# Optimization experiments

Measured on AMD Instinct MI355X. Metric: run time of the kernel, lower is better.

Reference implementation:

```python
import jax, jax.numpy as jnp
import numpy as np

B, N, C_IN, G = 8, 65536, 16, 64
CH = [16, 16]
EPS = 1e-3  # keras BatchNormalization default epsilon
OFFSETS = [(dx, dy, dz) for dx in (-1, 0, 1) for dy in (-1, 0, 1) for dz in (-1, 0, 1)]
G3 = G * G * G


def setup_inputs() -> dict:
    key = jax.random.key(0)
    k = jax.random.split(key, 8)
    voxel_features = jax.random.normal(k[0], (B, N, C_IN), dtype=jnp.float32)
    # unique active voxel coordinates per example (submanifold sites)
    lin = jax.vmap(lambda kk: jax.random.permutation(kk, G3)[:N])(jax.random.split(k[1], B))
    xyz = jnp.stack([lin // (G * G), (lin // G) % G, lin % G], axis=-1).astype(jnp.int32)
    num_valid_voxels = jax.random.randint(k[2], (B,), N // 2, N + 1).astype(jnp.int32)
    w0 = jax.random.uniform(k[3], (3, 3, 3, C_IN, CH[0]), minval=-0.05, maxval=0.05, dtype=jnp.float32)
    w1 = jax.random.uniform(k[4], (3, 3, 3, CH[0], CH[1]), minval=-0.05, maxval=0.05, dtype=jnp.float32)
    nw0 = jax.random.uniform(k[5], (3, 3, 3, 1, 1), minval=-0.05, maxval=0.05, dtype=jnp.float32)
    nw1 = jax.random.uniform(k[6], (3, 3, 3, 1, 1), minval=-0.05, maxval=0.05, dtype=jnp.float32)
    gamma0 = jnp.ones((CH[0],), jnp.float32); beta0 = jnp.zeros((CH[0],), jnp.float32)
    gamma1 = jnp.ones((CH[1],), jnp.float32); beta1 = jnp.zeros((CH[1],), jnp.float32)
    return dict(voxel_features=voxel_features, voxel_xyz_indices=xyz,
                num_valid_voxels=num_valid_voxels, w0=w0, w1=w1, nw0=nw0, nw1=nw1,
                gamma0=gamma0, beta0=beta0, gamma1=gamma1, beta1=beta1)


def build_neighbor_idx(coords, valid_mask):
    """For each voxel and each 3x3x3 offset, the row index of the active neighbor, or -1."""
    lin = coords[..., 0] * (G * G) + coords[..., 1] * G + coords[..., 2]  # [B,N]
    # invalid (padded) voxels write to a spare slot so they never match as neighbors
    write_lin = jnp.where(valid_mask, lin, G3 + 1)
    idx_map = jnp.full((B, G3 + 2), -1, jnp.int32)
    idx_map = idx_map.at[jnp.arange(B)[:, None], write_lin].set(
        jnp.broadcast_to(jnp.arange(N, dtype=jnp.int32)[None, :], (B, N)))
    brow = jnp.arange(B)[:, None]
    nb = []
    for dx, dy, dz in OFFSETS:
        nx = coords[..., 0] + dx; ny = coords[..., 1] + dy; nz = coords[..., 2] + dz
        inb = (nx >= 0) & (nx < G) & (ny >= 0) & (ny < G) & (nz >= 0) & (nz < G)
        nlin = jnp.where(inb, nx * (G * G) + ny * G + nz, G3)  # slot G3 always -1
        nb.append(idx_map[brow, nlin])
    return jnp.stack(nb, axis=1)  # [B,27,N]


def sparse_conv(feats, nb_idx, valid_mask, w):
    """Submanifold sparse 3D conv: output only at active sites, gathering active neighbors."""
    wf = w.reshape(27, w.shape[3], w.shape[4])  # offsets enumerate kernel taps in order
    out = jnp.zeros((feats.shape[0], feats.shape[1], w.shape[4]), feats.dtype)
    for o in range(27):
        idx = nb_idx[:, o]  # [B,N]
        g = jnp.take_along_axis(feats, jnp.maximum(idx, 0)[..., None], axis=1)
        g = jnp.where((idx >= 0)[..., None], g, 0.0)
        out = out + jnp.einsum('bnc,co->bno', g, wf[o])
    return out * valid_mask[..., None]


def masked_bn(x, valid_mask, num_valid, gamma, beta):
    m = valid_mask[..., None].astype(x.dtype)
    cnt = jnp.sum(num_valid).astype(x.dtype)
    mean = jnp.sum(x * m, axis=(0, 1)) / cnt
    var = jnp.sum(m * jnp.square(x - mean), axis=(0, 1)) / cnt
    xn = (x - mean) * jax.lax.rsqrt(var + EPS) * gamma + beta
    return xn * m  # padded rows are zero-padded, as in the TF layer


def reference(voxel_features, voxel_xyz_indices, num_valid_voxels,
              w0, w1, nw0, nw1, gamma0, beta0, gamma1, beta1):
    valid_mask = jnp.arange(N)[None, :] < num_valid_voxels[:, None]  # [B,N]
    nb_idx = build_neighbor_idx(voxel_xyz_indices, valid_mask)
    ones = jnp.ones((B, N, 1), jnp.float32)
    net = voxel_features
    for w, nw, g, b in ((w0, nw0, gamma0, beta0), (w1, nw1, gamma1, beta1)):
        net = sparse_conv(net, nb_idx, valid_mask, w)
        net_norm = sparse_conv(ones, nb_idx, valid_mask, nw)
        net = net / (1.0 + jnp.abs(net_norm))
        net = masked_bn(net, valid_mask, num_valid_voxels, g, b)
        net = jax.nn.relu(net)
    return net
```

## Files before the change

kernel.cpp:

```cpp
#include <hip/hip_runtime.h>
#include <cstdint>
#include <cstddef>

#define NB 8
#define NN 65536
#define NS (NN + 16)
#define GG 64
#define GG3 (GG*GG*GG)
#define NW (GG3/32)
#define NBLKC 2048
#define NP32 (NB * 2048)
#define EPSC 1e-3f

typedef __bf16 bf16x8 __attribute__((ext_vector_type(8)));
typedef float  f32x4  __attribute__((ext_vector_type(4)));

__device__ __forceinline__ unsigned short f2bf(float f) {
    unsigned u = __builtin_bit_cast(unsigned, f);
    unsigned r = (u + 0x7fffu + ((u >> 16) & 1u)) >> 16;
    return (unsigned short)r;
}
__device__ __forceinline__ unsigned pk2(float a, float b) {
    return (unsigned)f2bf(a) | ((unsigned)f2bf(b) << 16);
}
__device__ __forceinline__ float bf2f(unsigned short s) {
    return __builtin_bit_cast(float, (unsigned)s << 16);
}

__device__ __forceinline__ int site_rank2(const int2* __restrict__ mwb, int lin) {
    int2 mw = mwb[lin >> 5];
    uint32_t w = (uint32_t)mw.x;
    uint32_t bit = 1u << (lin & 31);
    if (!(w & bit)) return -1;
    return mw.y + __popc(w & (bit - 1u));
}

__global__ __launch_bounds__(256) void build_mask_kernel(
    const int* __restrict__ xyz, const int* __restrict__ nvv,
    uint32_t* __restrict__ mask,
    const float* __restrict__ w0, const float* __restrict__ w1,
    unsigned short* __restrict__ wf)
{
    int b = blockIdx.y;
    int n = blockIdx.x * 256 + threadIdx.x;
    if (n < nvv[b]) {
        const int* cp = xyz + ((size_t)b * NN + n) * 3;
        int lin = cp[0] * (GG * GG) + cp[1] * GG + cp[2];
        atomicOr(&mask[b * NW + (lin >> 5)], 1u << (lin & 31));
    }
    if (blockIdx.x == 0 && b < 2) {
        const float* w = b ? w1 : w0;
        unsigned short* o = wf + b * 14 * 512;
        for (int idx = threadIdx.x; idx < 14 * 512; idx += 256) {
            int i = idx >> 9;
            int rem = idx & 511;
            int L = rem >> 3, j = rem & 7;
            int quad = L >> 4, nn = L & 15;
            int off = 2 * i + (quad >> 1);
            int c = ((quad & 1) << 3) + j;
            float v = (off < 27) ? w[(off * 16 + c) * 16 + nn] : 0.f;
            o[idx] = f2bf(v);
        }
    }
}

__global__ __launch_bounds__(256) void scan_mask_kernel(
    const uint32_t* __restrict__ mask, int2* __restrict__ mwb)
{
    int b = blockIdx.x;
    const uint32_t* mb = mask + (size_t)b * NW;
    int2* wb = mwb + (size_t)b * NW;
    int t = threadIdx.x;

    uint32_t wv[32];
    int cnts[32];
    int local = 0;
    #pragma unroll
    for (int i = 0; i < 32; i++) {
        wv[i] = mb[t * 32 + i];
        cnts[i] = __popc(wv[i]);
        local += cnts[i];
    }

    __shared__ int sc[256];
    sc[t] = local;
    __syncthreads();
    for (int off = 1; off < 256; off <<= 1) {
        int v = (t >= off) ? sc[t - off] : 0;
        __syncthreads();
        sc[t] += v;
        __syncthreads();
    }
    int base = sc[t] - local;
    #pragma unroll
    for (int i = 0; i < 32; i++) {
        wb[t * 32 + i] = make_int2((int)wv[i], base);
        base += cnts[i];
    }
}

__global__ __launch_bounds__(256) void perm_gather_kernel(
    const int* __restrict__ xyz, const int* __restrict__ nvv,
    const int2* __restrict__ mwb,
    const float* __restrict__ feats,
    int2* __restrict__ srow,
    unsigned short* __restrict__ sfeats)
{
    int b = blockIdx.y;
    int n = blockIdx.x * 256 + threadIdx.x;
    int cnt = nvv[b];
    unsigned short* sfb = sfeats + (size_t)b * NS * 16;
    if (blockIdx.x == 0 && threadIdx.x < 16)
        sfb[(size_t)NN * 16 + threadIdx.x] = 0;
    if (n < cnt) {
        const int* cp = xyz + ((size_t)b * NN + n) * 3;
        int lin = cp[0] * (GG * GG) + cp[1] * GG + cp[2];
        int r = site_rank2(mwb + (size_t)b * NW, lin);
        srow[(size_t)b * NN + r] = make_int2(lin, n);
        const float4* fp = (const float4*)(feats + ((size_t)b * NN + n) * 16);
        float4 f0 = fp[0], f1 = fp[1], f2 = fp[2], f3 = fp[3];
        uint4 lo = make_uint4(pk2(f0.x, f0.y), pk2(f0.z, f0.w),
                              pk2(f1.x, f1.y), pk2(f1.z, f1.w));
        uint4 hi = make_uint4(pk2(f2.x, f2.y), pk2(f2.z, f2.w),
                              pk2(f3.x, f3.y), pk2(f3.z, f3.w));
        *(uint4*)(sfb + (size_t)r * 16)     = lo;
        *(uint4*)(sfb + (size_t)r * 16 + 8) = hi;
    } else {
        uint4 z = make_uint4(0, 0, 0, 0);
        *(uint4*)(sfb + (size_t)n * 16)     = z;
        *(uint4*)(sfb + (size_t)n * 16 + 8) = z;
    }
}

__global__ __launch_bounds__(256, 4) void conv_mfma_kernel(
    const unsigned short* __restrict__ sfeats,
    const int2*     __restrict__ srow,
    const int*      __restrict__ nvv,
    const int2*     __restrict__ mwb,
    const unsigned short* __restrict__ wfrag,
    const float*    __restrict__ nw,
    unsigned short* __restrict__ outbuf,
    float*          __restrict__ stats)
{
    int lane = threadIdx.x & 63;
    int wv = threadIdx.x >> 6;
    int m = lane & 15, quad = lane >> 4;
    int v = lane & 31, h = lane >> 5;
    int wid = blockIdx.x * 4 + wv;

    __shared__ int   jj[4][32][29];
    __shared__ float obuf[4][32][17];
    __shared__ float rrl[4][32];
    __shared__ float red[4][32];
    __shared__ float lnw[27];

    if (threadIdx.x < 27) lnw[threadIdx.x] = nw[threadIdx.x];

    bf16x8 bfr[14];
    #pragma unroll
    for (int i = 0; i < 14; i++)
        bfr[i] = *(const bf16x8*)(wfrag + i * 512 + lane * 8);
    __syncthreads();

    float psum = 0.f, psq = 0.f;
    int coff = (quad & 1) << 3;

    for (int pb = wid; pb < NP32; pb += 4 * NBLKC) {
        int b = pb >> 11;
        int r0 = (pb & 2047) << 5;
        int cnt = nvv[b];
        if (r0 >= cnt) continue;

        const int2* mb = mwb + (size_t)b * NW;
        const unsigned short* fb = sfeats + (size_t)b * NS * 16;
        const int2* sr = srow + (size_t)b * NN;

        int Rv = r0 + v;
        bool vld = Rv < cnt;
        int lin = vld ? sr[Rv].x : 0;
        int x = lin >> 12, y = (lin >> 6) & 63, z = lin & 63;
        int zb = z & 31;
        float nc = 0.f;
        #pragma unroll
        for (int t = 0; t < 5; t++) {
            int c = 2 * t + h;
            bool cok = c < 9;
            int cc = cok ? c : 0;
            int dx = cc / 3 - 1, dy = cc % 3 - 1;
            int nx = x + dx, ny = y + dy;
            bool colok = cok & ((unsigned)nx < 64u) & ((unsigned)ny < 64u);
            int wdi = colok ? (((nx << 12) + (ny << 6) + z) >> 5) : 0;

            int2 mw = make_int2(0, 0);
            if (vld & colok) mw = mb[wdi];
            bool need2 = vld & colok & (((zb == 0) & (z > 0)) | ((zb == 31) & (z < 63)));
            int w2 = wdi + ((zb == 0) ? -1 : 1);
            int2 mw2 = make_int2(0, 0);
            if (need2) mw2 = mb[w2];

            #pragma unroll
            for (int dz = -1; dz <= 1; dz++) {
                int zz = z + dz;
                bool zok = (unsigned)zz < 64u;
                bool same = (dz == 0) | ((dz < 0) ? (zb != 0) : (zb != 31));
                int2 word = same ? mw : mw2;
                int bb = zz & 31;
                uint32_t wm = (uint32_t)word.x;
                bool hit = vld & colok & zok & ((wm >> bb) & 1u);
                int rnk = word.y + __popc(wm & ((1u << bb) - 1u));
                int off = cc * 3 + dz + 1;
                int jv = hit ? rnk : NN;
                if (cok) {
                    jj[wv][v][off] = jv;
                    nc += hit ? lnw[off] : 0.f;
                }
            }
        }
        nc += __shfl_xor(nc, 32, 64);
        if (lane < 32) rrl[wv][v] = 1.f / (1.f + fabsf(nc));

        f32x4 acc0 = {0.f, 0.f, 0.f, 0.f};
        f32x4 acc1 = {0.f, 0.f, 0.f, 0.f};
        #pragma unroll
        for (int i = 0; i < 14; i++) {
            int off = 2 * i + (quad >> 1);
            int idx = off < 27 ? off : 28;
            int j0 = jj[wv][m][idx];      j0 = (off < 27) ? j0 : NN;
            int j1 = jj[wv][m + 16][idx]; j1 = (off < 27) ? j1 : NN;
            bf16x8 a0 = *(const bf16x8*)(fb + (size_t)j0 * 16 + coff);
            bf16x8 a1 = *(const bf16x8*)(fb + (size_t)j1 * 16 + coff);
            acc0 = __builtin_amdgcn_mfma_f32_16x16x32_bf16(a0, bfr[i], acc0, 0, 0, 0);
            acc1 = __builtin_amdgcn_mfma_f32_16x16x32_bf16(a1, bfr[i], acc1, 0, 0, 0);
        }

        #pragma unroll
        for (int hh = 0; hh < 2; hh++) {
            #pragma unroll
            for (int r4 = 0; r4 < 4; r4++) {
                int row = (hh << 4) + (quad << 2) + r4;
                float tval = (hh ? acc1[r4] : acc0[r4]) * rrl[wv][row];
                psum += tval; psq += tval * tval;
                obuf[wv][row][m] = tval;
            }
        }
        {
            int orow = v;
            int Rr = r0 + orow;
            if (Rr < cnt) {
                const float* src = &obuf[wv][orow][h * 8];
                uint4 val = make_uint4(pk2(src[0], src[1]), pk2(src[2], src[3]),
                                       pk2(src[4], src[5]), pk2(src[6], src[7]));
                *(uint4*)(outbuf + ((size_t)b * NN + Rr) * 16 + h * 8) = val;
            }
        }
    }

    psum += __shfl_xor(psum, 16, 64); psum += __shfl_xor(psum, 32, 64);
    psq  += __shfl_xor(psq, 16, 64);  psq  += __shfl_xor(psq, 32, 64);
    if (lane < 16) { red[wv][lane] = psum; red[wv][16 + lane] = psq; }
    __syncthreads();
    if (threadIdx.x < 32) {
        float vv = red[0][threadIdx.x] + red[1][threadIdx.x] +
                   red[2][threadIdx.x] + red[3][threadIdx.x];
        atomicAdd(&stats[(blockIdx.x & 15) * 32 + threadIdx.x], vv);
    }
}

__device__ __forceinline__ void compute_sb(
    const float* __restrict__ stats, const int* __restrict__ nvv,
    const float* __restrict__ gamma, const float* __restrict__ beta,
    float* sbs , float* sums )
{
    int tid = threadIdx.x;
    if (tid < 32) {
        float v = 0.f;
        #pragma unroll
        for (int s = 0; s < 16; s++) v += stats[s * 32 + tid];
        sums[tid] = v;
    }
    __syncthreads();
    if (tid < 16) {
        float cnt = 0.f;
        #pragma unroll
        for (int b = 0; b < NB; b++) cnt += (float)nvv[b];
        float mean = sums[tid] / cnt;
        float var  = fmaxf(sums[16 + tid] / cnt - mean * mean, 0.f);
        float scv = gamma[tid] * rsqrtf(var + EPSC);
        sbs[tid]      = scv;
        sbs[16 + tid] = beta[tid] - mean * scv;
    }
    __syncthreads();
}

__global__ __launch_bounds__(256) void bnrelu_sorted_kernel(
    const unsigned short* __restrict__ in, const float* __restrict__ stats,
    const int* __restrict__ nvv,
    const float* __restrict__ gamma, const float* __restrict__ beta,
    unsigned short* __restrict__ outb)
{
    __shared__ float sbs[32];
    __shared__ float sums[32];
    compute_sb(stats, nvv, gamma, beta, sbs, sums);

    int b = blockIdx.y;
    int r = blockIdx.x * 256 + threadIdx.x;
    if (r > NN) return;
    int cnt = nvv[b];
    uint4 lo = make_uint4(0, 0, 0, 0), hi = lo;
    if (r < cnt) {
        const uint4* ip = (const uint4*)(in + ((size_t)b * NN + r) * 16);
        uint4 xl = ip[0], xh = ip[1];
        float y[16];
        #pragma unroll
        for (int c = 0; c < 16; c++) {
            unsigned u = (c < 8) ? ((const unsigned*)&xl)[c >> 1]
                                 : ((const unsigned*)&xh)[(c - 8) >> 1];
            unsigned short sv = (c & 1) ? (unsigned short)(u >> 16)
                                        : (unsigned short)(u & 0xffff);
            y[c] = fmaxf(fmaf(bf2f(sv), sbs[c], sbs[16 + c]), 0.f);
        }
        lo = make_uint4(pk2(y[0], y[1]), pk2(y[2], y[3]), pk2(y[4], y[5]), pk2(y[6], y[7]));
        hi = make_uint4(pk2(y[8], y[9]), pk2(y[10], y[11]), pk2(y[12], y[13]), pk2(y[14], y[15]));
    }
    unsigned short* op = outb + ((size_t)b * NS + r) * 16;
    *(uint4*)op       = lo;
    *(uint4*)(op + 8) = hi;
}

__global__ __launch_bounds__(256) void final_scatter_kernel(
    const unsigned short* __restrict__ in,
    const int2* __restrict__ srow,
    const float* __restrict__ stats, const int* __restrict__ nvv,
    const float* __restrict__ gamma, const float* __restrict__ beta,
    float* __restrict__ out)
{
    __shared__ float sbs[32];
    __shared__ float sums[32];
    compute_sb(stats, nvv, gamma, beta, sbs, sums);

    int b = blockIdx.y;
    int r = blockIdx.x * 256 + threadIdx.x;
    int cnt = nvv[b];
    if (r < cnt) {
        const uint4* ip = (const uint4*)(in + ((size_t)b * NN + r) * 16);
        uint4 xl = ip[0], xh = ip[1];
        float y[16];
        #pragma unroll
        for (int c = 0; c < 16; c++) {
            unsigned u = (c < 8) ? ((const unsigned*)&xl)[c >> 1]
                                 : ((const unsigned*)&xh)[(c - 8) >> 1];
            unsigned short sv = (c & 1) ? (unsigned short)(u >> 16)
                                        : (unsigned short)(u & 0xffff);
            y[c] = fmaxf(fmaf(bf2f(sv), sbs[c], sbs[16 + c]), 0.f);
        }
        int n = srow[(size_t)b * NN + r].y;
        float4* op = (float4*)(out + ((size_t)b * NN + n) * 16);
        op[0] = make_float4(y[0],  y[1],  y[2],  y[3]);
        op[1] = make_float4(y[4],  y[5],  y[6],  y[7]);
        op[2] = make_float4(y[8],  y[9],  y[10], y[11]);
        op[3] = make_float4(y[12], y[13], y[14], y[15]);
    } else {
        float4 z = make_float4(0.f, 0.f, 0.f, 0.f);
        float4* op = (float4*)(out + ((size_t)b * NN + r) * 16);
        op[0] = z; op[1] = z; op[2] = z; op[3] = z;
    }
}

extern "C" void kernel_launch(void* const* d_in, const int* in_sizes, int n_in,
                              void* d_out, int out_size, void* d_ws, size_t ws_size,
                              hipStream_t stream)
{
    const float* feats  = (const float*)d_in[0];
    const int*   xyz    = (const int*)d_in[1];
    const int*   nvv    = (const int*)d_in[2];
    const float* w0     = (const float*)d_in[3];
    const float* w1     = (const float*)d_in[4];
    const float* nw0    = (const float*)d_in[5];
    const float* nw1    = (const float*)d_in[6];
    const float* gamma0 = (const float*)d_in[7];
    const float* beta0  = (const float*)d_in[8];
    const float* gamma1 = (const float*)d_in[9];
    const float* beta1  = (const float*)d_in[10];
    float* out = (float*)d_out;

    char* ws = (char*)d_ws;
    uint32_t* mask    = (uint32_t*)ws;       ws += (size_t)NB * NW * 4;
    float*    stats1  = (float*)ws;          ws += 16 * 32 * 4;
    float*    stats2  = (float*)ws;          ws += 16 * 32 * 4;
    int2*     mwb     = (int2*)ws;           ws += (size_t)NB * NW * 8;
    int2*     srow    = (int2*)ws;           ws += (size_t)NB * NN * 8;
    unsigned short* sfA = (unsigned short*)ws; ws += (size_t)NB * NS * 16 * 2;
    unsigned short* sfB = (unsigned short*)ws; ws += (size_t)NB * NS * 16 * 2;
    unsigned short* bufPre = (unsigned short*)ws; ws += (size_t)NB * NN * 16 * 2;
    unsigned short* wfr = (unsigned short*)ws; ws += (size_t)2 * 14 * 512 * 2;

    hipMemsetAsync(mask, 0, (size_t)NB * NW * 4 + 16 * 32 * 4 * 2, stream);

    dim3 gridBN(NN / 256, NB);
    build_mask_kernel<<<gridBN, 256, 0, stream>>>(xyz, nvv, mask, w0, w1, wfr);
    scan_mask_kernel<<<NB, 256, 0, stream>>>(mask, mwb);
    perm_gather_kernel<<<gridBN, 256, 0, stream>>>(xyz, nvv, mwb, feats, srow, sfA);

    conv_mfma_kernel<<<NBLKC, 256, 0, stream>>>(
        sfA, srow, nvv, mwb, wfr, nw0, bufPre, stats1);
    bnrelu_sorted_kernel<<<dim3(NN / 256 + 1, NB), 256, 0, stream>>>(
        bufPre, stats1, nvv, gamma0, beta0, sfB);

    conv_mfma_kernel<<<NBLKC, 256, 0, stream>>>(
        sfB, srow, nvv, mwb, wfr + 14 * 512, nw1, bufPre, stats2);

    final_scatter_kernel<<<dim3(NN / 256, NB), 256, 0, stream>>>(
        bufPre, srow, stats2, nvv, gamma1, beta1, out);
}
```

Measured before the change: 241.0 us.

## Compact conv work list over valid rows and make BN in place

The conv kernel now iterates over a compacted list of only the valid 32-row tiles across batches, using prefix sums of per-batch counts, and runs on a smaller grid. Before, it strided over all tiles and skipped the empty ones, which left waves idle. Linear coordinates are computed once in build_mask and reused by the gather step. The separate pre-BN buffer is dropped: conv writes into the ping-pong buffers, BN+ReLU runs in place, and the zero padding writes for invalid rows are removed, since only the sentinel row at NN is zeroed now. This relies on gathered neighbour indices never touching rows at or beyond the count except the sentinel.

```diff
diff --git a/kernel.cpp b/kernel.cpp
--- a/kernel.cpp
+++ b/kernel.cpp
@@ -8,8 +8,7 @@
 #define GG 64
 #define GG3 (GG*GG*GG)
 #define NW (GG3/32)
-#define NBLKC 2048
-#define NP32 (NB * 2048)
+#define NBLKC 1536
 #define EPSC 1e-3f
 
 typedef __bf16 bf16x8 __attribute__((ext_vector_type(8)));
@@ -37,7 +36,7 @@
 
 __global__ __launch_bounds__(256) void build_mask_kernel(
     const int* __restrict__ xyz, const int* __restrict__ nvv,
-    uint32_t* __restrict__ mask,
+    uint32_t* __restrict__ mask, int* __restrict__ linb,
     const float* __restrict__ w0, const float* __restrict__ w1,
     unsigned short* __restrict__ wf)
 {
@@ -46,6 +45,7 @@
     if (n < nvv[b]) {
         const int* cp = xyz + ((size_t)b * NN + n) * 3;
         int lin = cp[0] * (GG * GG) + cp[1] * GG + cp[2];
+        linb[(size_t)b * NN + n] = lin;
         atomicOr(&mask[b * NW + (lin >> 5)], 1u << (lin & 31));
     }
     if (blockIdx.x == 0 && b < 2) {
@@ -100,7 +100,7 @@
 }
 
 __global__ __launch_bounds__(256) void perm_gather_kernel(
-    const int* __restrict__ xyz, const int* __restrict__ nvv,
+    const int* __restrict__ linb, const int* __restrict__ nvv,
     const int2* __restrict__ mwb,
     const float* __restrict__ feats,
     int2* __restrict__ srow,
@@ -113,8 +113,7 @@
     if (blockIdx.x == 0 && threadIdx.x < 16)
         sfb[(size_t)NN * 16 + threadIdx.x] = 0;
     if (n < cnt) {
-        const int* cp = xyz + ((size_t)b * NN + n) * 3;
-        int lin = cp[0] * (GG * GG) + cp[1] * GG + cp[2];
+        int lin = linb[(size_t)b * NN + n];
         int r = site_rank2(mwb + (size_t)b * NW, lin);
         srow[(size_t)b * NN + r] = make_int2(lin, n);
         const float4* fp = (const float4*)(feats + ((size_t)b * NN + n) * 16);
@@ -125,10 +124,6 @@
                               pk2(f3.x, f3.y), pk2(f3.z, f3.w));
         *(uint4*)(sfb + (size_t)r * 16)     = lo;
         *(uint4*)(sfb + (size_t)r * 16 + 8) = hi;
-    } else {
-        uint4 z = make_uint4(0, 0, 0, 0);
-        *(uint4*)(sfb + (size_t)n * 16)     = z;
-        *(uint4*)(sfb + (size_t)n * 16 + 8) = z;
     }
 }
 
@@ -156,6 +151,15 @@
 
     if (threadIdx.x < 27) lnw[threadIdx.x] = nw[threadIdx.x];
 
+    int cnts[8], cum[9];
+    cum[0] = 0;
+    #pragma unroll
+    for (int b = 0; b < 8; b++) {
+        cnts[b] = nvv[b];
+        cum[b + 1] = cum[b] + ((cnts[b] + 31) >> 5);
+    }
+    int total = cum[8];
+
     bf16x8 bfr[14];
     #pragma unroll
     for (int i = 0; i < 14; i++)
@@ -165,11 +169,12 @@
     float psum = 0.f, psq = 0.f;
     int coff = (quad & 1) << 3;
 
-    for (int pb = wid; pb < NP32; pb += 4 * NBLKC) {
-        int b = pb >> 11;
-        int r0 = (pb & 2047) << 5;
-        int cnt = nvv[b];
-        if (r0 >= cnt) continue;
+    for (int vp = wid; vp < total; vp += 4 * NBLKC) {
+        int b = 0;
+        #pragma unroll
+        for (int k = 1; k < 8; k++) b += (vp >= cum[k]);
+        int r0 = (vp - cum[b]) << 5;
+        int cnt = cnts[b];
 
         const int2* mb = mwb + (size_t)b * NW;
         const unsigned short* fb = sfeats + (size_t)b * NS * 16;
@@ -244,13 +249,12 @@
             }
         }
         {
-            int orow = v;
-            int Rr = r0 + orow;
+            int Rr = r0 + v;
             if (Rr < cnt) {
-                const float* src = &obuf[wv][orow][h * 8];
+                const float* src = &obuf[wv][v][h * 8];
                 uint4 val = make_uint4(pk2(src[0], src[1]), pk2(src[2], src[3]),
                                        pk2(src[4], src[5]), pk2(src[6], src[7]));
-                *(uint4*)(outbuf + ((size_t)b * NN + Rr) * 16 + h * 8) = val;
+                *(uint4*)(outbuf + ((size_t)b * NS + Rr) * 16 + h * 8) = val;
             }
         }
     }
@@ -293,10 +297,9 @@
 }
 
 __global__ __launch_bounds__(256) void bnrelu_sorted_kernel(
-    const unsigned short* __restrict__ in, const float* __restrict__ stats,
+    unsigned short* __restrict__ buf, const float* __restrict__ stats,
     const int* __restrict__ nvv,
-    const float* __restrict__ gamma, const float* __restrict__ beta,
-    unsigned short* __restrict__ outb)
+    const float* __restrict__ gamma, const float* __restrict__ beta)
 {
     __shared__ float sbs[32];
     __shared__ float sums[32];
@@ -306,10 +309,9 @@
     int r = blockIdx.x * 256 + threadIdx.x;
     if (r > NN) return;
     int cnt = nvv[b];
-    uint4 lo = make_uint4(0, 0, 0, 0), hi = lo;
+    unsigned short* op = buf + ((size_t)b * NS + r) * 16;
     if (r < cnt) {
-        const uint4* ip = (const uint4*)(in + ((size_t)b * NN + r) * 16);
-        uint4 xl = ip[0], xh = ip[1];
+        uint4 xl = *(const uint4*)op, xh = *(const uint4*)(op + 8);
         float y[16];
         #pragma unroll
         for (int c = 0; c < 16; c++) {
@@ -319,12 +321,15 @@
                                         : (unsigned short)(u & 0xffff);
             y[c] = fmaxf(fmaf(bf2f(sv), sbs[c], sbs[16 + c]), 0.f);
         }
-        lo = make_uint4(pk2(y[0], y[1]), pk2(y[2], y[3]), pk2(y[4], y[5]), pk2(y[6], y[7]));
-        hi = make_uint4(pk2(y[8], y[9]), pk2(y[10], y[11]), pk2(y[12], y[13]), pk2(y[14], y[15]));
-    }
-    unsigned short* op = outb + ((size_t)b * NS + r) * 16;
-    *(uint4*)op       = lo;
-    *(uint4*)(op + 8) = hi;
+        *(uint4*)op       = make_uint4(pk2(y[0], y[1]), pk2(y[2], y[3]),
+                                       pk2(y[4], y[5]), pk2(y[6], y[7]));
+        *(uint4*)(op + 8) = make_uint4(pk2(y[8], y[9]), pk2(y[10], y[11]),
+                                       pk2(y[12], y[13]), pk2(y[14], y[15]));
+    } else if (r == NN) {
+        uint4 z = make_uint4(0, 0, 0, 0);
+        *(uint4*)op       = z;
+        *(uint4*)(op + 8) = z;
+    }
 }
 
 __global__ __launch_bounds__(256) void final_scatter_kernel(
@@ -342,7 +347,7 @@
     int r = blockIdx.x * 256 + threadIdx.x;
     int cnt = nvv[b];
     if (r < cnt) {
-        const uint4* ip = (const uint4*)(in + ((size_t)b * NN + r) * 16);
+        const uint4* ip = (const uint4*)(in + ((size_t)b * NS + r) * 16);
         uint4 xl = ip[0], xh = ip[1];
         float y[16];
         #pragma unroll
@@ -389,26 +394,26 @@
     float*    stats2  = (float*)ws;          ws += 16 * 32 * 4;
     int2*     mwb     = (int2*)ws;           ws += (size_t)NB * NW * 8;
     int2*     srow    = (int2*)ws;           ws += (size_t)NB * NN * 8;
+    int*      linb    = (int*)ws;            ws += (size_t)NB * NN * 4;
     unsigned short* sfA = (unsigned short*)ws; ws += (size_t)NB * NS * 16 * 2;
     unsigned short* sfB = (unsigned short*)ws; ws += (size_t)NB * NS * 16 * 2;
-    unsigned short* bufPre = (unsigned short*)ws; ws += (size_t)NB * NN * 16 * 2;
     unsigned short* wfr = (unsigned short*)ws; ws += (size_t)2 * 14 * 512 * 2;
 
     hipMemsetAsync(mask, 0, (size_t)NB * NW * 4 + 16 * 32 * 4 * 2, stream);
 
     dim3 gridBN(NN / 256, NB);
-    build_mask_kernel<<<gridBN, 256, 0, stream>>>(xyz, nvv, mask, w0, w1, wfr);
+    build_mask_kernel<<<gridBN, 256, 0, stream>>>(xyz, nvv, mask, linb, w0, w1, wfr);
     scan_mask_kernel<<<NB, 256, 0, stream>>>(mask, mwb);
-    perm_gather_kernel<<<gridBN, 256, 0, stream>>>(xyz, nvv, mwb, feats, srow, sfA);
+    perm_gather_kernel<<<gridBN, 256, 0, stream>>>(linb, nvv, mwb, feats, srow, sfA);
 
     conv_mfma_kernel<<<NBLKC, 256, 0, stream>>>(
-        sfA, srow, nvv, mwb, wfr, nw0, bufPre, stats1);
+        sfA, srow, nvv, mwb, wfr, nw0, sfB, stats1);
     bnrelu_sorted_kernel<<<dim3(NN / 256 + 1, NB), 256, 0, stream>>>(
-        bufPre, stats1, nvv, gamma0, beta0, sfB);
+        sfB, stats1, nvv, gamma0, beta0);
 
     conv_mfma_kernel<<<NBLKC, 256, 0, stream>>>(
-        sfB, srow, nvv, mwb, wfr + 14 * 512, nw1, bufPre, stats2);
+        sfB, srow, nvv, mwb, wfr + 14 * 512, nw1, sfA, stats2);
 
     final_scatter_kernel<<<dim3(NN / 256, NB), 256, 0, stream>>>(
-        bufPre, srow, stats2, nvv, gamma1, beta1, out);
-}
+        sfA, srow, stats2, nvv, gamma1, beta1, out);
+}
```

New measurement: 256.8 us. 6.6% more time.
